# Optimization experiments

Hardware: AMD Instinct MI355X
Metric: run time of the kernel (lower is better)

The kernel has to match this reference:

```python
import jax, jax.numpy as jnp
import numpy as np

E = 128  # embed_size


def setup_inputs() -> dict:
    key = jax.random.key(0)
    ks = jax.random.split(key, 20)
    NU, NI, NEV = 100000, 50000, 4096
    s = 0.05  # weight scale so softplus(dot) stays well-conditioned
    inp = {
        "user_emb": jax.random.normal(ks[0], (NU, E), jnp.float32) * s,
        "item_emb": jax.random.normal(ks[1], (NI, E), jnp.float32) * s,
        "ugru_wi": jax.random.normal(ks[2], (3 * E, E), jnp.float32) * s,
        "ugru_wh": jax.random.normal(ks[3], (3 * E, E), jnp.float32) * s,
        "ugru_bi": jax.random.normal(ks[4], (3 * E,), jnp.float32) * s,
        "ugru_bh": jax.random.normal(ks[5], (3 * E,), jnp.float32) * s,
        "igru_wi": jax.random.normal(ks[6], (3 * E, E), jnp.float32) * s,
        "igru_wh": jax.random.normal(ks[7], (3 * E, E), jnp.float32) * s,
        "igru_bi": jax.random.normal(ks[8], (3 * E,), jnp.float32) * s,
        "igru_bh": jax.random.normal(ks[9], (3 * E,), jnp.float32) * s,
        "t1_w": jax.random.normal(ks[10], (E, 2 * E), jnp.float32) * s,
        "t1_b": jax.random.normal(ks[11], (E,), jnp.float32) * s,
        "t2_w": jax.random.normal(ks[12], (32, E), jnp.float32) * s,
        "t2_b": jax.random.normal(ks[13], (32,), jnp.float32) * s,
        "t3_w": jax.random.normal(ks[14], (1, 32), jnp.float32) * s,
        "t3_b": jax.random.normal(ks[15], (1,), jnp.float32) * s,
        "user_ids": jax.random.randint(ks[16], (NEV,), 0, NU, jnp.int32),
        "item_ids": jax.random.randint(ks[17], (NEV,), 0, NI, jnp.int32),
    }
    return inp


def _gru(x, h, wi, wh, bi, bh):
    # torch.nn.GRUCell math, single sample: x,h [E]; wi,wh [3E,E]
    gi = wi @ x + bi
    gh = wh @ h + bh
    ir, iz, inn = jnp.split(gi, 3)
    hr, hz, hn = jnp.split(gh, 3)
    r = jax.nn.sigmoid(ir + hr)
    z = jax.nn.sigmoid(iz + hz)
    n = jnp.tanh(inn + r * hn)
    return (1.0 - z) * n + z * h


def reference(user_emb, item_emb, ugru_wi, ugru_wh, ugru_bi, ugru_bh,
              igru_wi, igru_wh, igru_bi, igru_bh,
              t1_w, t1_b, t2_w, t2_b, t3_w, t3_b,
              user_ids, item_ids):
    # Sequential event processing: per-event gather of user/item embedding,
    # Rayleigh base compatibility score, MLP (transForm1/2/3) branch score,
    # coupled GRUCell updates scattered back into the embedding tables.
    def step(carry, ev):
        U, V = carry
        u_id, i_id = ev
        u = U[u_id]          # [E] gather (dict-cache lookup in original)
        v = V[i_id]          # [E]
        comp = jax.nn.softplus(jnp.dot(u, v)) + 1e-10  # base_compatibility
        loss = -jnp.log(comp)                           # -log p(event)
        cat = jnp.concatenate([u, v])                   # [2E]
        h = jax.nn.relu(t1_w @ cat + t1_b)              # transForm1 + act
        h = jax.nn.relu(t2_w @ h + t2_b)                # transForm2 + act
        score = jax.nn.sigmoid(t3_w @ h + t3_b)[0]      # transForm3
        nu = _gru(v, u, ugru_wi, ugru_wh, ugru_bi, ugru_bh)  # user_cell
        nv = _gru(u, v, igru_wi, igru_wh, igru_bi, igru_bh)  # item_cell
        U = U.at[u_id].set(nu)  # coevolution scatter
        V = V.at[i_id].set(nv)
        return (U, V), jnp.stack([loss, score])

    (_, _), outs = jax.lax.scan(step, (user_emb, item_emb),
                                (user_ids, item_ids))
    return outs  # [num_events, 2] : (-log comp, branch score)
```

## Files before the change

kernel.cpp:

```cpp
#include <hip/hip_runtime.h>
#include <math.h>

#define EMB 128
#define MAXEV 4096
#define GEV 16

struct Hdr { int nl0; int nl1; int ncomp2; };

typedef __attribute__((ext_vector_type(8))) short bf16x8;
typedef __attribute__((ext_vector_type(4))) float f32x4;

__device__ __forceinline__ float sigmoidf_(float x) { return 1.0f / (1.0f + expf(-x)); }
__device__ __forceinline__ float softplusf_(float x) {
    return (x > 0.f) ? x + log1pf(expf(-x)) : log1pf(expf(x));
}
__device__ __forceinline__ unsigned short f2bf(float f) {
    unsigned int u = __float_as_uint(f);
    u += 0x7FFFu + ((u >> 16) & 1u);
    return (unsigned short)(u >> 16);
}
__device__ __forceinline__ float bf2f(unsigned short s) {
    return __uint_as_float((unsigned int)s << 16);
}

__global__ __launch_bounds__(64) void prev_kernel(
    const int* __restrict__ uids, const int* __restrict__ iids,
    int* __restrict__ prevu, int* __restrict__ previ, int nev)
{
    int t = blockIdx.x;
    if (t >= nev) return;
    int lane = threadIdx.x;
    int myu = uids[t], myi = iids[t];
    int bu = -1, bi = -1;
    for (int j = lane; j < t; j += 64) {
        if (uids[j] == myu) bu = j;
        if (iids[j] == myi) bi = j;
    }
    for (int off = 32; off; off >>= 1) {
        bu = max(bu, __shfl_xor(bu, off));
        bi = max(bi, __shfl_xor(bi, off));
    }
    if (lane == 0) { prevu[t] = bu; previ[t] = bi; }
}

__global__ __launch_bounds__(1024) void setup_kernel(
    const int* __restrict__ prevu, const int* __restrict__ previ,
    int* __restrict__ order0, int* __restrict__ order1,
    int* __restrict__ tail2Order, int* __restrict__ compStart,
    Hdr* __restrict__ hdr, int nev)
{
    __shared__ int   lab[MAXEV];
    __shared__ int   tmpT[MAXEV];
    __shared__ int   skey[MAXEV];
    __shared__ short slev[MAXEV];
    __shared__ int   schanged, sn0, sn1, sn2;

    int tid = threadIdx.x;
    for (int t = tid; t < nev; t += 1024) { lab[t] = t; slev[t] = 0; }
    if (tid == 0) { sn0 = 0; sn1 = 0; sn2 = 0; }
    __syncthreads();

    for (int it = 0; it < nev; ++it) {
        if (tid == 0) schanged = 0;
        __syncthreads();
        for (int t = tid; t < nev; t += 1024) {
            int pu = prevu[t], pi = previ[t];
            int nl = 0;
            if (pu >= 0) nl = slev[pu] + 1;
            if (pi >= 0) { int c = slev[pi] + 1; nl = nl > c ? nl : c; }
            if (nl > (int)slev[t]) { slev[t] = (short)nl; schanged = 1; }
        }
        __syncthreads();
        if (!schanged) break;
        __syncthreads();
    }

    for (int it = 0; it < nev; ++it) {
        if (tid == 0) schanged = 0;
        __syncthreads();
        for (int t = tid; t < nev; t += 1024) {
            int m = lab[t];
            int pu = prevu[t], pi = previ[t];
            if (pu >= 0) m = min(m, lab[pu]);
            if (pi >= 0) m = min(m, lab[pi]);
            if (m < lab[t]) { atomicMin(&lab[t], m); schanged = 1; }
            if (pu >= 0 && m < lab[pu]) { atomicMin(&lab[pu], m); schanged = 1; }
            if (pi >= 0 && m < lab[pi]) { atomicMin(&lab[pi], m); schanged = 1; }
        }
        __syncthreads();
        if (!schanged) break;
        __syncthreads();
    }

    for (int t = tid; t < nev; t += 1024) {
        int l = slev[t];
        if (l == 0)      order0[atomicAdd(&sn0, 1)] = t;
        else if (l == 1) order1[atomicAdd(&sn1, 1)] = t;
        else             tmpT[atomicAdd(&sn2, 1)] = t;
    }
    __syncthreads();
    int n2 = sn2;

    for (int i = tid; i < n2; i += 1024)
        skey[i] = (lab[tmpT[i]] << 12) | tmpT[i];
    __syncthreads();

    for (int i = tid; i < n2; i += 1024) {
        int k = skey[i], r = 0;
        for (int j = 0; j < n2; ++j) r += (skey[j] < k);
        tail2Order[r] = tmpT[i];
        lab[r] = k;
    }
    __syncthreads();

    if (tid == 0) {
        int nc = 0;
        for (int i = 0; i < n2; ++i)
            if (i == 0 || (lab[i] >> 12) != (lab[i - 1] >> 12))
                compStart[nc++] = i;
        compStart[nc] = n2;
        hdr->nl0 = sn0;
        hdr->nl1 = sn1;
        hdr->ncomp2 = nc;
    }
}

__global__ __launch_bounds__(256) void wcvt_kernel(
    const float* __restrict__ Wuh, const float* __restrict__ Wii,
    const float* __restrict__ Wui, const float* __restrict__ Wih,
    const float* __restrict__ T1w,
    unsigned short* __restrict__ wb_uh, unsigned short* __restrict__ wb_ii,
    unsigned short* __restrict__ wb_ui, unsigned short* __restrict__ wb_ih,
    unsigned short* __restrict__ t1wb)
{
    int m = blockIdx.y;
    const float* src = (m == 0) ? Wuh : (m == 1) ? Wii : (m == 2) ? Wui
                      : (m == 3) ? Wih : T1w;
    unsigned short* dst = (m == 0) ? wb_uh : (m == 1) ? wb_ii : (m == 2) ? wb_ui
                        : (m == 3) ? wb_ih : t1wb;
    int nf4 = (m < 4) ? (384 * EMB / 4) : (EMB * 256 / 4);
    int q = blockIdx.x * 256 + threadIdx.x;
    if (q >= nf4) return;
    float4 v = ((const float4*)src)[q];
    ushort4 o = make_ushort4(f2bf(v.x), f2bf(v.y), f2bf(v.z), f2bf(v.w));
    *(ushort4*)(dst + (size_t)q * 4) = o;
}

__global__ __launch_bounds__(256) void gru_fused_kernel(
    const float* __restrict__ U0, const float* __restrict__ V0,
    const unsigned short* __restrict__ wb_ui, const unsigned short* __restrict__ wb_uh,
    const unsigned short* __restrict__ wb_ii, const unsigned short* __restrict__ wb_ih,
    const float* __restrict__ bui, const float* __restrict__ buh,
    const float* __restrict__ bii, const float* __restrict__ bih,
    const int* __restrict__ uids, const int* __restrict__ iids,
    const int* __restrict__ prevu, const int* __restrict__ previ,
    const float* NUr, const float* NVr,
    const int* __restrict__ order, const int* __restrict__ cnt_p,
    float* NU, float* NV)
{
    __shared__ __align__(16) unsigned short xbu[GEV][EMB];
    __shared__ __align__(16) unsigned short xbv[GEV][EMB];
    __shared__ float gg[GEV][772];

    int cnt = *cnt_p;
    int e0 = blockIdx.x * GEV;
    if (e0 >= cnt) return;

    int tid = threadIdx.x;
    int ev = tid >> 4, c8 = (tid & 15) * 8;

    {
        int e = e0 + ev;
        float4 a0, a1, c0, c1;
        if (e < cnt) {
            int t = order[e];
            int pu = prevu[t], pi = previ[t];
            const float* up = (pu < 0 ? U0 + (size_t)uids[t] * EMB : NUr + (size_t)pu * EMB) + c8;
            const float* vp = (pi < 0 ? V0 + (size_t)iids[t] * EMB : NVr + (size_t)pi * EMB) + c8;
            a0 = ((const float4*)up)[0]; a1 = ((const float4*)up)[1];
            c0 = ((const float4*)vp)[0]; c1 = ((const float4*)vp)[1];
        } else {
            a0 = make_float4(0.f, 0.f, 0.f, 0.f); a1 = a0; c0 = a0; c1 = a0;
        }
        *(ushort4*)&xbu[ev][c8]     = make_ushort4(f2bf(a0.x), f2bf(a0.y), f2bf(a0.z), f2bf(a0.w));
        *(ushort4*)&xbu[ev][c8 + 4] = make_ushort4(f2bf(a1.x), f2bf(a1.y), f2bf(a1.z), f2bf(a1.w));
        *(ushort4*)&xbv[ev][c8]     = make_ushort4(f2bf(c0.x), f2bf(c0.y), f2bf(c0.z), f2bf(c0.w));
        *(ushort4*)&xbv[ev][c8 + 4] = make_ushort4(f2bf(c1.x), f2bf(c1.y), f2bf(c1.z), f2bf(c1.w));
    }
    __syncthreads();

    int w = tid >> 6, l = tid & 63;
    int lr = l & 15, lk = (l >> 4) * 8;

    for (int ph = 0; ph < 2; ++ph) {
        const unsigned short* Wi = ph ? wb_ii : wb_ui;
        const unsigned short* Wh = ph ? wb_ih : wb_uh;
        const unsigned short (*Xi)[EMB] = ph ? xbu : xbv;
        const unsigned short (*Xh)[EMB] = ph ? xbv : xbu;

        f32x4 acc[12] = {};
        #pragma unroll
        for (int kk = 0; kk < 4; ++kk) {
            bf16x8 ai = *(const bf16x8*)&Xi[lr][kk * 32 + lk];
            bf16x8 ah = *(const bf16x8*)&Xh[lr][kk * 32 + lk];
            #pragma unroll
            for (int j = 0; j < 12; ++j) {
                int nt = w * 12 + j;
                bool ish = nt >= 24;
                int brow = (ish ? nt - 24 : nt) * 16 + lr;
                const unsigned short* W = ish ? Wh : Wi;
                bf16x8 b = *(const bf16x8*)(W + (size_t)brow * EMB + kk * 32 + lk);
                acc[j] = __builtin_amdgcn_mfma_f32_16x16x32_bf16(ish ? ah : ai, b, acc[j], 0, 0, 0);
            }
        }
        #pragma unroll
        for (int j = 0; j < 12; ++j) {
            int nt = w * 12 + j;
            #pragma unroll
            for (int i = 0; i < 4; ++i)
                gg[(l >> 4) * 4 + i][nt * 16 + lr] = acc[j][i];
        }
        __syncthreads();

        {
            int e = e0 + ev;
            if (e < cnt) {
                int t = order[e];
                const float* bi = ph ? bii : bui;
                const float* bh = ph ? bih : buh;
                float* N = ph ? NV : NU;
                const unsigned short (*xh)[EMB] = ph ? xbv : xbu;
                #pragma unroll
                for (int i = 0; i < 8; ++i) {
                    int ch = c8 + i;
                    float r_ = sigmoidf_(gg[ev][ch] + bi[ch] + gg[ev][384 + ch] + bh[ch]);
                    float z_ = sigmoidf_(gg[ev][128 + ch] + bi[128 + ch] + gg[ev][512 + ch] + bh[128 + ch]);
                    float n_ = tanhf(gg[ev][256 + ch] + bi[256 + ch] + r_ * (gg[ev][640 + ch] + bh[256 + ch]));
                    float h = bf2f(xh[ev][ch]);
                    N[(size_t)t * EMB + ch] = (1.f - z_) * n_ + z_ * h;
                }
            }
        }
        __syncthreads();
    }
}

__global__ __launch_bounds__(1024) void tail2_kernel(
    const float* __restrict__ U0,  const float* __restrict__ V0,
    const float* __restrict__ Wui, const float* __restrict__ Wuh,
    const float* __restrict__ bui, const float* __restrict__ buh,
    const float* __restrict__ Wii, const float* __restrict__ Wih,
    const float* __restrict__ bii, const float* __restrict__ bih,
    const int* __restrict__ uids,  const int* __restrict__ iids,
    const int* __restrict__ prevu, const int* __restrict__ previ,
    const int* __restrict__ tail2Order, const int* __restrict__ compStart,
    const Hdr* __restrict__ hdr,
    float* __restrict__ NU, float* __restrict__ NV)
{
    __shared__ __align__(16) float su[EMB];
    __shared__ __align__(16) float sv[EMB];
    __shared__ float gg[1536];
    int tid = threadIdx.x;
    int ncomp = hdr->ncomp2;

    int g = tid >> 4, j = tid & 15;
    int mat = g >> 4;
    const float* W = (mat == 0) ? Wui : (mat == 1) ? Wuh : (mat == 2) ? Wii : Wih;

    for (int c = blockIdx.x; c < ncomp; c += gridDim.x) {
        int kb = compStart[c], ke = compStart[c + 1];
        for (int k = kb; k < ke; ++k) {
            int t = tail2Order[k];
            int pu = prevu[t], pi = previ[t];
            const float* up = (pu < 0) ? U0 + (size_t)uids[t] * EMB : NU + (size_t)pu * EMB;
            const float* vp = (pi < 0) ? V0 + (size_t)iids[t] * EMB : NV + (size_t)pi * EMB;
            __syncthreads();
            if (tid < EMB)        su[tid] = up[tid];
            else if (tid < 2*EMB) sv[tid - EMB] = vp[tid - EMB];
            __syncthreads();

            const float* x = (mat == 1 || mat == 2) ? su : sv;
            const float4* x4 = (const float4*)x;
            float4 xa = x4[2 * j], xb = x4[2 * j + 1];
            #pragma unroll 1
            for (int b = 0; b < 3; ++b) {
                int rbase = (g & 15) * 24 + b * 8;
                float4 w0[8], w1[8];
                #pragma unroll
                for (int q = 0; q < 8; ++q) {
                    const float4* W4 = (const float4*)(W + (size_t)(rbase + q) * EMB);
                    w0[q] = W4[2 * j]; w1[q] = W4[2 * j + 1];
                }
                #pragma unroll
                for (int q = 0; q < 8; ++q) {
                    float s = w0[q].x * xa.x + w0[q].y * xa.y
                            + w0[q].z * xa.z + w0[q].w * xa.w
                            + w1[q].x * xb.x + w1[q].y * xb.y
                            + w1[q].z * xb.z + w1[q].w * xb.w;
                    s += __shfl_xor(s, 1); s += __shfl_xor(s, 2);
                    s += __shfl_xor(s, 4); s += __shfl_xor(s, 8);
                    if (j == q) gg[mat * 384 + rbase + q] = s;
                }
            }
            __syncthreads();

            if (tid < EMB) {
                int e = tid;
                float r_ = sigmoidf_(gg[e] + bui[e] + gg[384 + e] + buh[e]);
                float z_ = sigmoidf_(gg[128 + e] + bui[128 + e] + gg[512 + e] + buh[128 + e]);
                float n_ = tanhf(gg[256 + e] + bui[256 + e] + r_ * (gg[640 + e] + buh[256 + e]));
                NU[(size_t)t * EMB + e] = (1.f - z_) * n_ + z_ * su[e];
            } else if (tid < 2*EMB) {
                int e = tid - EMB;
                float r_ = sigmoidf_(gg[768 + e] + bii[e] + gg[1152 + e] + bih[e]);
                float z_ = sigmoidf_(gg[896 + e] + bii[128 + e] + gg[1280 + e] + bih[128 + e]);
                float n_ = tanhf(gg[1024 + e] + bii[256 + e] + r_ * (gg[1408 + e] + bih[256 + e]));
                NV[(size_t)t * EMB + e] = (1.f - z_) * n_ + z_ * sv[e];
            }
        }
    }
}

__global__ __launch_bounds__(256) void gatherall_kernel(
    const float* __restrict__ U0, const float* __restrict__ V0,
    const int* __restrict__ uids, const int* __restrict__ iids,
    const int* __restrict__ prevu, const int* __restrict__ previ,
    const float* __restrict__ NU, const float* __restrict__ NV,
    unsigned short* __restrict__ XAub, unsigned short* __restrict__ XAvb,
    float* __restrict__ out, int nev)
{
    int sub = threadIdx.x >> 5;
    int lane = threadIdx.x & 31;
    int t = blockIdx.x * 8 + sub;
    if (t >= nev) return;
    int pu = prevu[t], pi = previ[t];
    const float4* up = (const float4*)(pu < 0 ?
        U0 + (size_t)uids[t] * EMB : NU + (size_t)pu * EMB);
    const float4* vp = (const float4*)(pi < 0 ?
        V0 + (size_t)iids[t] * EMB : NV + (size_t)pi * EMB);
    float4 a = up[lane], c = vp[lane];
    *(ushort4*)(XAub + (size_t)t * EMB + lane * 4) =
        make_ushort4(f2bf(a.x), f2bf(a.y), f2bf(a.z), f2bf(a.w));
    *(ushort4*)(XAvb + (size_t)t * EMB + lane * 4) =
        make_ushort4(f2bf(c.x), f2bf(c.y), f2bf(c.z), f2bf(c.w));
    float dp = a.x * c.x + a.y * c.y + a.z * c.z + a.w * c.w;
    dp += __shfl_xor(dp, 1); dp += __shfl_xor(dp, 2);
    dp += __shfl_xor(dp, 4); dp += __shfl_xor(dp, 8);
    dp += __shfl_xor(dp, 16);
    if (lane == 0) out[2 * (size_t)t] = -logf(softplusf_(dp) + 1e-10f);
}

__global__ __launch_bounds__(256) void t1_mfma_kernel(
    const unsigned short* __restrict__ XAub, const unsigned short* __restrict__ XAvb,
    const unsigned short* __restrict__ t1wb, const float* __restrict__ T1b,
    float* __restrict__ H1, int nev)
{
    int ev0 = blockIdx.x * 64;
    int row0 = blockIdx.y * 64;
    int tid = threadIdx.x;
    int w = tid >> 6, l = tid & 63;
    int lr = l & 15, lk = (l >> 4) * 8;
    int erow = ev0 + w * 16 + lr;

    f32x4 acc[4] = {};
    #pragma unroll
    for (int kh = 0; kh < 8; ++kh) {
        const unsigned short* Xb = (kh < 4) ? XAub : XAvb;
        bf16x8 a = *(const bf16x8*)(Xb + (size_t)erow * EMB + (kh & 3) * 32 + lk);
        #pragma unroll
        for (int n = 0; n < 4; ++n) {
            bf16x8 b = *(const bf16x8*)(t1wb + (size_t)(row0 + n * 16 + lr) * 256 + kh * 32 + lk);
            acc[n] = __builtin_amdgcn_mfma_f32_16x16x32_bf16(a, b, acc[n], 0, 0, 0);
        }
    }
    int drow = ev0 + w * 16 + (l >> 4) * 4;
    #pragma unroll
    for (int n = 0; n < 4; ++n) {
        int col = row0 + n * 16 + lr;
        float bb = T1b[col];
        #pragma unroll
        for (int i = 0; i < 4; ++i)
            H1[(size_t)(drow + i) * EMB + col] = fmaxf(acc[n][i] + bb, 0.f);
    }
}

__global__ __launch_bounds__(256) void t2t3_kernel(
    const float* __restrict__ H1,
    const float* __restrict__ T2w, const float* __restrict__ T2b,
    const float* __restrict__ T3w, const float* __restrict__ T3b,
    float* __restrict__ out, int nev)
{
    __shared__ __align__(16) float w2s[32][132];
    __shared__ __align__(16) float h1s[16][132];
    __shared__ float h2s[16][36];
    int tid = threadIdx.x;
    int ev = tid >> 4, j = tid & 15;
    int t = blockIdx.x * 16 + ev;

    {
        const float4* s2 = (const float4*)T2w;
        #pragma unroll
        for (int i = 0; i < 4; ++i) {
            int q = i * 256 + tid;
            int r = q >> 5, c4 = q & 31;
            *(float4*)&w2s[r][c4 * 4] = s2[q];
        }
    }
    {
        const float4* h4 = (const float4*)(H1 + (size_t)(blockIdx.x * 16 + ev) * EMB);
        *(float4*)&h1s[ev][8 * j]     = h4[2 * j];
        *(float4*)&h1s[ev][8 * j + 4] = h4[2 * j + 1];
    }
    __syncthreads();

    float acc0 = T2b[2 * j], acc1 = T2b[2 * j + 1];
    const float4* wr0 = (const float4*)&w2s[2 * j][0];
    const float4* wr1 = (const float4*)&w2s[2 * j + 1][0];
    const float4* xh = (const float4*)&h1s[ev][0];
    #pragma unroll
    for (int k = 0; k < 32; ++k) {
        float4 x = xh[k], a = wr0[k], b = wr1[k];
        acc0 = fmaf(a.x, x.x, acc0); acc0 = fmaf(a.y, x.y, acc0);
        acc0 = fmaf(a.z, x.z, acc0); acc0 = fmaf(a.w, x.w, acc0);
        acc1 = fmaf(b.x, x.x, acc1); acc1 = fmaf(b.y, x.y, acc1);
        acc1 = fmaf(b.z, x.z, acc1); acc1 = fmaf(b.w, x.w, acc1);
    }
    h2s[ev][2 * j]     = fmaxf(acc0, 0.f);
    h2s[ev][2 * j + 1] = fmaxf(acc1, 0.f);
    __syncthreads();

    float p = T3w[2 * j] * h2s[ev][2 * j] + T3w[2 * j + 1] * h2s[ev][2 * j + 1];
    p += __shfl_xor(p, 1); p += __shfl_xor(p, 2);
    p += __shfl_xor(p, 4); p += __shfl_xor(p, 8);
    if (j == 0 && t < nev)
        out[2 * (size_t)t + 1] = sigmoidf_(p + T3b[0]);
}

extern "C" void kernel_launch(void* const* d_in, const int* in_sizes, int n_in,
                              void* d_out, int out_size, void* d_ws, size_t ws_size,
                              hipStream_t stream)
{
    const float* U0  = (const float*)d_in[0];
    const float* V0  = (const float*)d_in[1];
    const float* Wui = (const float*)d_in[2];
    const float* Wuh = (const float*)d_in[3];
    const float* bui = (const float*)d_in[4];
    const float* buh = (const float*)d_in[5];
    const float* Wii = (const float*)d_in[6];
    const float* Wih = (const float*)d_in[7];
    const float* bii = (const float*)d_in[8];
    const float* bih = (const float*)d_in[9];
    const float* T1w = (const float*)d_in[10];
    const float* T1b = (const float*)d_in[11];
    const float* T2w = (const float*)d_in[12];
    const float* T2b = (const float*)d_in[13];
    const float* T3w = (const float*)d_in[14];
    const float* T3b = (const float*)d_in[15];
    const int* uids  = (const int*)d_in[16];
    const int* iids  = (const int*)d_in[17];
    int nev = in_sizes[16];

    char* ws = (char*)d_ws;
    int* base = (int*)ws;
    int* prevu      = base;
    int* previ      = base + MAXEV;
    int* order0     = base + 2 * MAXEV;
    int* order1     = base + 3 * MAXEV;
    int* tail2Order = base + 4 * MAXEV;
    int* compStart  = base + 5 * MAXEV;
    Hdr* hdr        = (Hdr*)(base + 6 * MAXEV + 4);
    float* NU = (float*)(ws + (160 << 10));
    float* NV = NU + (size_t)MAXEV * EMB;
    float* Xu = NV + (size_t)MAXEV * EMB;
    float* Xv = Xu + (size_t)MAXEV * EMB;
    float* Gu = Xv + (size_t)MAXEV * EMB;
    float* Gv = Gu + (size_t)MAXEV * 768;
    unsigned short* Xub = (unsigned short*)(Gv + (size_t)MAXEV * 768);
    unsigned short* Xvb = Xub + (size_t)MAXEV * EMB;
    unsigned short* wb_uh = Xvb + (size_t)MAXEV * EMB;
    unsigned short* wb_ii = wb_uh + 384 * EMB;
    unsigned short* wb_ui = wb_ii + 384 * EMB;
    unsigned short* wb_ih = wb_ui + 384 * EMB;
    unsigned short* t1wb  = wb_ih + 384 * EMB;
    float* out = (float*)d_out;

    prev_kernel<<<nev, 64, 0, stream>>>(uids, iids, prevu, previ, nev);
    wcvt_kernel<<<dim3(48, 5), 256, 0, stream>>>(
        Wuh, Wii, Wui, Wih, T1w, wb_uh, wb_ii, wb_ui, wb_ih, t1wb);
    setup_kernel<<<1, 1024, 0, stream>>>(prevu, previ, order0, order1,
                                         tail2Order, compStart, hdr, nev);

    gru_fused_kernel<<<MAXEV / GEV, 256, 0, stream>>>(
        U0, V0, wb_ui, wb_uh, wb_ii, wb_ih, bui, buh, bii, bih,
        uids, iids, prevu, previ, NU, NV, order0, &hdr->nl0, NU, NV);

    gru_fused_kernel<<<MAXEV / GEV, 256, 0, stream>>>(
        U0, V0, wb_ui, wb_uh, wb_ii, wb_ih, bui, buh, bii, bih,
        uids, iids, prevu, previ, NU, NV, order1, &hdr->nl1, NU, NV);

    tail2_kernel<<<64, 1024, 0, stream>>>(
        U0, V0, Wui, Wuh, bui, buh, Wii, Wih, bii, bih,
        uids, iids, prevu, previ, tail2Order, compStart, hdr, NU, NV);

    unsigned short* XAub = Xub;
    unsigned short* XAvb = Xvb;
    float* H1 = Gu;
    gatherall_kernel<<<(nev + 7) / 8, 256, 0, stream>>>(
        U0, V0, uids, iids, prevu, previ, NU, NV, XAub, XAvb, out, nev);
    t1_mfma_kernel<<<dim3((nev + 63) / 64, 2), 256, 0, stream>>>(
        XAub, XAvb, t1wb, T1b, H1, nev);
    t2t3_kernel<<<(nev + 15) / 16, 256, 0, stream>>>(
        H1, T2w, T2b, T3w, T3b, out, nev);
}
```

Before: 122.6 us.

## Fuse weight conversion into prev kernel, fuse post MLP kernels, prune setup work

Weight bf16 conversion, now including T2w, is folded into prev_kernel, which removes one launch. The gather, T1 MFMA, T2 and T3 stages become a single post_fused_kernel that keeps activations in LDS and uses MFMA for T2, so the H1 and X round trips through global memory go away. setup_kernel now runs level propagation only over events that have predecessors and labelling only over tail events, and it drops one shared array. GRU LDS rows are padded to 136 to reduce bank conflicts. T2 now runs in bf16, which trades some precision for speed.

```diff
diff --git a/kernel.cpp b/kernel.cpp
--- a/kernel.cpp
+++ b/kernel.cpp
@@ -25,11 +25,34 @@
 
 __global__ __launch_bounds__(64) void prev_kernel(
     const int* __restrict__ uids, const int* __restrict__ iids,
-    int* __restrict__ prevu, int* __restrict__ previ, int nev)
+    int* __restrict__ prevu, int* __restrict__ previ, int nev,
+    const float* __restrict__ Wuh, const float* __restrict__ Wii,
+    const float* __restrict__ Wui, const float* __restrict__ Wih,
+    const float* __restrict__ T1w, const float* __restrict__ T2w,
+    unsigned short* __restrict__ wb_uh, unsigned short* __restrict__ wb_ii,
+    unsigned short* __restrict__ wb_ui, unsigned short* __restrict__ wb_ih,
+    unsigned short* __restrict__ t1wb, unsigned short* __restrict__ t2wb)
 {
     int t = blockIdx.x;
+    int lane = threadIdx.x;
+
+    {
+        int gid = t * 64 + lane;
+        if (gid < 58368) {
+            const float* src; unsigned short* dst; int q;
+            if (gid < 49152) {
+                int m = gid / 12288; q = gid - m * 12288;
+                src = (m == 0) ? Wuh : (m == 1) ? Wii : (m == 2) ? Wui : Wih;
+                dst = (m == 0) ? wb_uh : (m == 1) ? wb_ii : (m == 2) ? wb_ui : wb_ih;
+            } else if (gid < 57344) { q = gid - 49152; src = T1w; dst = t1wb; }
+            else                    { q = gid - 57344; src = T2w; dst = t2wb; }
+            float4 v = ((const float4*)src)[q];
+            *(ushort4*)(dst + (size_t)q * 4) =
+                make_ushort4(f2bf(v.x), f2bf(v.y), f2bf(v.z), f2bf(v.w));
+        }
+    }
+
     if (t >= nev) return;
-    int lane = threadIdx.x;
     int myu = uids[t], myi = iids[t];
     int bu = -1, bi = -1;
     for (int j = lane; j < t; j += 64) {
@@ -51,19 +74,27 @@
 {
     __shared__ int   lab[MAXEV];
     __shared__ int   tmpT[MAXEV];
-    __shared__ int   skey[MAXEV];
+    __shared__ int   t2l[MAXEV];
     __shared__ short slev[MAXEV];
-    __shared__ int   schanged, sn0, sn1, sn2;
+    __shared__ int   schanged, sn0, sn1, sn2, sntl;
 
     int tid = threadIdx.x;
-    for (int t = tid; t < nev; t += 1024) { lab[t] = t; slev[t] = 0; }
-    if (tid == 0) { sn0 = 0; sn1 = 0; sn2 = 0; }
-    __syncthreads();
+    for (int t = tid; t < nev; t += 1024) slev[t] = 0;
+    if (tid == 0) { sn0 = 0; sn1 = 0; sn2 = 0; sntl = 0; }
+    __syncthreads();
+
+    for (int t = tid; t < nev; t += 1024) {
+        if (prevu[t] >= 0 || previ[t] >= 0) tmpT[atomicAdd(&sntl, 1)] = t;
+        else                                 order0[atomicAdd(&sn0, 1)] = t;
+    }
+    __syncthreads();
+    int ntl = sntl;
 
     for (int it = 0; it < nev; ++it) {
         if (tid == 0) schanged = 0;
         __syncthreads();
-        for (int t = tid; t < nev; t += 1024) {
+        for (int i = tid; i < ntl; i += 1024) {
+            int t = tmpT[i];
             int pu = prevu[t], pi = previ[t];
             int nl = 0;
             if (pu >= 0) nl = slev[pu] + 1;
@@ -75,75 +106,55 @@
         __syncthreads();
     }
 
+    for (int i = tid; i < ntl; i += 1024) {
+        int t = tmpT[i];
+        if (slev[t] == 1)      order1[atomicAdd(&sn1, 1)] = t;
+        else if (slev[t] >= 2) t2l[atomicAdd(&sn2, 1)] = t;
+    }
+    __syncthreads();
+    int n2 = sn2;
+
+    for (int i = tid; i < n2; i += 1024) lab[t2l[i]] = t2l[i];
+    __syncthreads();
     for (int it = 0; it < nev; ++it) {
         if (tid == 0) schanged = 0;
         __syncthreads();
-        for (int t = tid; t < nev; t += 1024) {
+        for (int i = tid; i < n2; i += 1024) {
+            int t = t2l[i];
             int m = lab[t];
             int pu = prevu[t], pi = previ[t];
-            if (pu >= 0) m = min(m, lab[pu]);
-            if (pi >= 0) m = min(m, lab[pi]);
+            bool eu = (pu >= 0 && slev[pu] >= 2);
+            bool ei = (pi >= 0 && slev[pi] >= 2);
+            if (eu) m = min(m, lab[pu]);
+            if (ei) m = min(m, lab[pi]);
             if (m < lab[t]) { atomicMin(&lab[t], m); schanged = 1; }
-            if (pu >= 0 && m < lab[pu]) { atomicMin(&lab[pu], m); schanged = 1; }
-            if (pi >= 0 && m < lab[pi]) { atomicMin(&lab[pi], m); schanged = 1; }
+            if (eu && m < lab[pu]) { atomicMin(&lab[pu], m); schanged = 1; }
+            if (ei && m < lab[pi]) { atomicMin(&lab[pi], m); schanged = 1; }
         }
         __syncthreads();
         if (!schanged) break;
         __syncthreads();
     }
 
-    for (int t = tid; t < nev; t += 1024) {
-        int l = slev[t];
-        if (l == 0)      order0[atomicAdd(&sn0, 1)] = t;
-        else if (l == 1) order1[atomicAdd(&sn1, 1)] = t;
-        else             tmpT[atomicAdd(&sn2, 1)] = t;
-    }
-    __syncthreads();
-    int n2 = sn2;
-
-    for (int i = tid; i < n2; i += 1024)
-        skey[i] = (lab[tmpT[i]] << 12) | tmpT[i];
-    __syncthreads();
-
+    for (int i = tid; i < n2; i += 1024) tmpT[i] = (lab[t2l[i]] << 12) | t2l[i];
+    __syncthreads();
     for (int i = tid; i < n2; i += 1024) {
-        int k = skey[i], r = 0;
-        for (int j = 0; j < n2; ++j) r += (skey[j] < k);
-        tail2Order[r] = tmpT[i];
-        lab[r] = k;
+        int k = tmpT[i], r = 0;
+        for (int j = 0; j < n2; ++j) r += (tmpT[j] < k);
+        tail2Order[r] = k & 0xFFF;
     }
     __syncthreads();
 
     if (tid == 0) {
         int nc = 0;
         for (int i = 0; i < n2; ++i)
-            if (i == 0 || (lab[i] >> 12) != (lab[i - 1] >> 12))
+            if (i == 0 || lab[tail2Order[i]] != lab[tail2Order[i - 1]])
                 compStart[nc++] = i;
         compStart[nc] = n2;
+        hdr->ncomp2 = nc;
         hdr->nl0 = sn0;
         hdr->nl1 = sn1;
-        hdr->ncomp2 = nc;
-    }
-}
-
-__global__ __launch_bounds__(256) void wcvt_kernel(
-    const float* __restrict__ Wuh, const float* __restrict__ Wii,
-    const float* __restrict__ Wui, const float* __restrict__ Wih,
-    const float* __restrict__ T1w,
-    unsigned short* __restrict__ wb_uh, unsigned short* __restrict__ wb_ii,
-    unsigned short* __restrict__ wb_ui, unsigned short* __restrict__ wb_ih,
-    unsigned short* __restrict__ t1wb)
-{
-    int m = blockIdx.y;
-    const float* src = (m == 0) ? Wuh : (m == 1) ? Wii : (m == 2) ? Wui
-                      : (m == 3) ? Wih : T1w;
-    unsigned short* dst = (m == 0) ? wb_uh : (m == 1) ? wb_ii : (m == 2) ? wb_ui
-                        : (m == 3) ? wb_ih : t1wb;
-    int nf4 = (m < 4) ? (384 * EMB / 4) : (EMB * 256 / 4);
-    int q = blockIdx.x * 256 + threadIdx.x;
-    if (q >= nf4) return;
-    float4 v = ((const float4*)src)[q];
-    ushort4 o = make_ushort4(f2bf(v.x), f2bf(v.y), f2bf(v.z), f2bf(v.w));
-    *(ushort4*)(dst + (size_t)q * 4) = o;
+    }
 }
 
 __global__ __launch_bounds__(256) void gru_fused_kernel(
@@ -158,8 +169,8 @@
     const int* __restrict__ order, const int* __restrict__ cnt_p,
     float* NU, float* NV)
 {
-    __shared__ __align__(16) unsigned short xbu[GEV][EMB];
-    __shared__ __align__(16) unsigned short xbv[GEV][EMB];
+    __shared__ __align__(16) unsigned short xbu[GEV][136];
+    __shared__ __align__(16) unsigned short xbv[GEV][136];
     __shared__ float gg[GEV][772];
 
     int cnt = *cnt_p;
@@ -195,8 +206,8 @@
     for (int ph = 0; ph < 2; ++ph) {
         const unsigned short* Wi = ph ? wb_ii : wb_ui;
         const unsigned short* Wh = ph ? wb_ih : wb_uh;
-        const unsigned short (*Xi)[EMB] = ph ? xbu : xbv;
-        const unsigned short (*Xh)[EMB] = ph ? xbv : xbu;
+        const unsigned short (*Xi)[136] = ph ? xbu : xbv;
+        const unsigned short (*Xh)[136] = ph ? xbv : xbu;
 
         f32x4 acc[12] = {};
         #pragma unroll
@@ -229,7 +240,7 @@
                 const float* bi = ph ? bii : bui;
                 const float* bh = ph ? bih : buh;
                 float* N = ph ? NV : NU;
-                const unsigned short (*xh)[EMB] = ph ? xbv : xbu;
+                const unsigned short (*xh)[136] = ph ? xbv : xbu;
                 #pragma unroll
                 for (int i = 0; i < 8; ++i) {
                     int ch = c8 + i;
@@ -321,119 +332,115 @@
     }
 }
 
-__global__ __launch_bounds__(256) void gatherall_kernel(
+__global__ __launch_bounds__(256) void post_fused_kernel(
     const float* __restrict__ U0, const float* __restrict__ V0,
     const int* __restrict__ uids, const int* __restrict__ iids,
     const int* __restrict__ prevu, const int* __restrict__ previ,
     const float* __restrict__ NU, const float* __restrict__ NV,
-    unsigned short* __restrict__ XAub, unsigned short* __restrict__ XAvb,
-    float* __restrict__ out, int nev)
-{
-    int sub = threadIdx.x >> 5;
-    int lane = threadIdx.x & 31;
-    int t = blockIdx.x * 8 + sub;
-    if (t >= nev) return;
-    int pu = prevu[t], pi = previ[t];
-    const float4* up = (const float4*)(pu < 0 ?
-        U0 + (size_t)uids[t] * EMB : NU + (size_t)pu * EMB);
-    const float4* vp = (const float4*)(pi < 0 ?
-        V0 + (size_t)iids[t] * EMB : NV + (size_t)pi * EMB);
-    float4 a = up[lane], c = vp[lane];
-    *(ushort4*)(XAub + (size_t)t * EMB + lane * 4) =
-        make_ushort4(f2bf(a.x), f2bf(a.y), f2bf(a.z), f2bf(a.w));
-    *(ushort4*)(XAvb + (size_t)t * EMB + lane * 4) =
-        make_ushort4(f2bf(c.x), f2bf(c.y), f2bf(c.z), f2bf(c.w));
-    float dp = a.x * c.x + a.y * c.y + a.z * c.z + a.w * c.w;
-    dp += __shfl_xor(dp, 1); dp += __shfl_xor(dp, 2);
-    dp += __shfl_xor(dp, 4); dp += __shfl_xor(dp, 8);
-    dp += __shfl_xor(dp, 16);
-    if (lane == 0) out[2 * (size_t)t] = -logf(softplusf_(dp) + 1e-10f);
-}
-
-__global__ __launch_bounds__(256) void t1_mfma_kernel(
-    const unsigned short* __restrict__ XAub, const unsigned short* __restrict__ XAvb,
     const unsigned short* __restrict__ t1wb, const float* __restrict__ T1b,
-    float* __restrict__ H1, int nev)
-{
-    int ev0 = blockIdx.x * 64;
-    int row0 = blockIdx.y * 64;
-    int tid = threadIdx.x;
-    int w = tid >> 6, l = tid & 63;
-    int lr = l & 15, lk = (l >> 4) * 8;
-    int erow = ev0 + w * 16 + lr;
-
-    f32x4 acc[4] = {};
-    #pragma unroll
-    for (int kh = 0; kh < 8; ++kh) {
-        const unsigned short* Xb = (kh < 4) ? XAub : XAvb;
-        bf16x8 a = *(const bf16x8*)(Xb + (size_t)erow * EMB + (kh & 3) * 32 + lk);
-        #pragma unroll
-        for (int n = 0; n < 4; ++n) {
-            bf16x8 b = *(const bf16x8*)(t1wb + (size_t)(row0 + n * 16 + lr) * 256 + kh * 32 + lk);
-            acc[n] = __builtin_amdgcn_mfma_f32_16x16x32_bf16(a, b, acc[n], 0, 0, 0);
-        }
-    }
-    int drow = ev0 + w * 16 + (l >> 4) * 4;
-    #pragma unroll
-    for (int n = 0; n < 4; ++n) {
-        int col = row0 + n * 16 + lr;
-        float bb = T1b[col];
-        #pragma unroll
-        for (int i = 0; i < 4; ++i)
-            H1[(size_t)(drow + i) * EMB + col] = fmaxf(acc[n][i] + bb, 0.f);
-    }
-}
-
-__global__ __launch_bounds__(256) void t2t3_kernel(
-    const float* __restrict__ H1,
-    const float* __restrict__ T2w, const float* __restrict__ T2b,
+    const unsigned short* __restrict__ t2wb, const float* __restrict__ T2b,
     const float* __restrict__ T3w, const float* __restrict__ T3b,
     float* __restrict__ out, int nev)
 {
-    __shared__ __align__(16) float w2s[32][132];
-    __shared__ __align__(16) float h1s[16][132];
-    __shared__ float h2s[16][36];
+    __shared__ __align__(16) unsigned short xau[64][136];
+    __shared__ __align__(16) unsigned short xav[64][136];
+    __shared__ __align__(16) unsigned short h1b[64][136];
+    __shared__ float h2s[64][36];
+
     int tid = threadIdx.x;
-    int ev = tid >> 4, j = tid & 15;
-    int t = blockIdx.x * 16 + ev;
+    int ev0 = blockIdx.x * 64;
+
+    #pragma unroll
+    for (int rep = 0; rep < 4; ++rep) {
+        int idx = rep * 256 + tid;
+        int evl = idx >> 4, j16 = idx & 15;
+        int t = ev0 + evl;
+        float4 a0, a1, c0, c1;
+        if (t < nev) {
+            int pu = prevu[t], pi = previ[t];
+            const float* up = (pu < 0 ? U0 + (size_t)uids[t] * EMB : NU + (size_t)pu * EMB) + j16 * 8;
+            const float* vp = (pi < 0 ? V0 + (size_t)iids[t] * EMB : NV + (size_t)pi * EMB) + j16 * 8;
+            a0 = ((const float4*)up)[0]; a1 = ((const float4*)up)[1];
+            c0 = ((const float4*)vp)[0]; c1 = ((const float4*)vp)[1];
+        } else {
+            a0 = make_float4(0.f, 0.f, 0.f, 0.f); a1 = a0; c0 = a0; c1 = a0;
+        }
+        *(ushort4*)&xau[evl][j16 * 8]     = make_ushort4(f2bf(a0.x), f2bf(a0.y), f2bf(a0.z), f2bf(a0.w));
+        *(ushort4*)&xau[evl][j16 * 8 + 4] = make_ushort4(f2bf(a1.x), f2bf(a1.y), f2bf(a1.z), f2bf(a1.w));
+        *(ushort4*)&xav[evl][j16 * 8]     = make_ushort4(f2bf(c0.x), f2bf(c0.y), f2bf(c0.z), f2bf(c0.w));
+        *(ushort4*)&xav[evl][j16 * 8 + 4] = make_ushort4(f2bf(c1.x), f2bf(c1.y), f2bf(c1.z), f2bf(c1.w));
+        float dp = a0.x * c0.x + a0.y * c0.y + a0.z * c0.z + a0.w * c0.w
+                 + a1.x * c1.x + a1.y * c1.y + a1.z * c1.z + a1.w * c1.w;
+        dp += __shfl_xor(dp, 1); dp += __shfl_xor(dp, 2);
+        dp += __shfl_xor(dp, 4); dp += __shfl_xor(dp, 8);
+        if (j16 == 0 && t < nev)
+            out[2 * (size_t)t] = -logf(softplusf_(dp) + 1e-10f);
+    }
+    __syncthreads();
+
+    int w = tid >> 6, l = tid & 63;
+    int lr = l & 15, lk = (l >> 4) * 8;
 
     {
-        const float4* s2 = (const float4*)T2w;
-        #pragma unroll
-        for (int i = 0; i < 4; ++i) {
-            int q = i * 256 + tid;
-            int r = q >> 5, c4 = q & 31;
-            *(float4*)&w2s[r][c4 * 4] = s2[q];
-        }
-    }
+        f32x4 acc[8] = {};
+        #pragma unroll
+        for (int kh = 0; kh < 8; ++kh) {
+            const unsigned short* ar = (kh < 4)
+                ? &xau[w * 16 + lr][kh * 32 + lk]
+                : &xav[w * 16 + lr][(kh - 4) * 32 + lk];
+            bf16x8 a = *(const bf16x8*)ar;
+            #pragma unroll
+            for (int n = 0; n < 8; ++n) {
+                bf16x8 b = *(const bf16x8*)(t1wb + (size_t)(n * 16 + lr) * 256 + kh * 32 + lk);
+                acc[n] = __builtin_amdgcn_mfma_f32_16x16x32_bf16(a, b, acc[n], 0, 0, 0);
+            }
+        }
+        #pragma unroll
+        for (int n = 0; n < 8; ++n) {
+            int col = n * 16 + lr;
+            float bb = T1b[col];
+            #pragma unroll
+            for (int i = 0; i < 4; ++i)
+                h1b[w * 16 + (l >> 4) * 4 + i][col] = f2bf(fmaxf(acc[n][i] + bb, 0.f));
+        }
+    }
+    __syncthreads();
+
     {
-        const float4* h4 = (const float4*)(H1 + (size_t)(blockIdx.x * 16 + ev) * EMB);
-        *(float4*)&h1s[ev][8 * j]     = h4[2 * j];
-        *(float4*)&h1s[ev][8 * j + 4] = h4[2 * j + 1];
-    }
-    __syncthreads();
-
-    float acc0 = T2b[2 * j], acc1 = T2b[2 * j + 1];
-    const float4* wr0 = (const float4*)&w2s[2 * j][0];
-    const float4* wr1 = (const float4*)&w2s[2 * j + 1][0];
-    const float4* xh = (const float4*)&h1s[ev][0];
-    #pragma unroll
-    for (int k = 0; k < 32; ++k) {
-        float4 x = xh[k], a = wr0[k], b = wr1[k];
-        acc0 = fmaf(a.x, x.x, acc0); acc0 = fmaf(a.y, x.y, acc0);
-        acc0 = fmaf(a.z, x.z, acc0); acc0 = fmaf(a.w, x.w, acc0);
-        acc1 = fmaf(b.x, x.x, acc1); acc1 = fmaf(b.y, x.y, acc1);
-        acc1 = fmaf(b.z, x.z, acc1); acc1 = fmaf(b.w, x.w, acc1);
-    }
-    h2s[ev][2 * j]     = fmaxf(acc0, 0.f);
-    h2s[ev][2 * j + 1] = fmaxf(acc1, 0.f);
-    __syncthreads();
-
-    float p = T3w[2 * j] * h2s[ev][2 * j] + T3w[2 * j + 1] * h2s[ev][2 * j + 1];
-    p += __shfl_xor(p, 1); p += __shfl_xor(p, 2);
-    p += __shfl_xor(p, 4); p += __shfl_xor(p, 8);
-    if (j == 0 && t < nev)
-        out[2 * (size_t)t + 1] = sigmoidf_(p + T3b[0]);
+        f32x4 acc2[2] = {};
+        #pragma unroll
+        for (int kk = 0; kk < 4; ++kk) {
+            bf16x8 a = *(const bf16x8*)&h1b[w * 16 + lr][kk * 32 + lk];
+            #pragma unroll
+            for (int n = 0; n < 2; ++n) {
+                bf16x8 b = *(const bf16x8*)(t2wb + (size_t)(n * 16 + lr) * 128 + kk * 32 + lk);
+                acc2[n] = __builtin_amdgcn_mfma_f32_16x16x32_bf16(a, b, acc2[n], 0, 0, 0);
+            }
+        }
+        #pragma unroll
+        for (int n = 0; n < 2; ++n) {
+            int col = n * 16 + lr;
+            float bb = T2b[col];
+            #pragma unroll
+            for (int i = 0; i < 4; ++i)
+                h2s[w * 16 + (l >> 4) * 4 + i][col] = fmaxf(acc2[n][i] + bb, 0.f);
+        }
+    }
+    __syncthreads();
+
+    {
+        int evl = tid >> 2, q4 = tid & 3;
+        float p = 0.f;
+        #pragma unroll
+        for (int i = 0; i < 8; ++i) {
+            int ch = q4 * 8 + i;
+            p = fmaf(T3w[ch], h2s[evl][ch], p);
+        }
+        p += __shfl_xor(p, 1); p += __shfl_xor(p, 2);
+        int t = ev0 + evl;
+        if (q4 == 0 && t < nev)
+            out[2 * (size_t)t + 1] = sigmoidf_(p + T3b[0]);
+    }
 }
 
 extern "C" void kernel_launch(void* const* d_in, const int* in_sizes, int n_in,
@@ -471,22 +478,18 @@
     Hdr* hdr        = (Hdr*)(base + 6 * MAXEV + 4);
     float* NU = (float*)(ws + (160 << 10));
     float* NV = NU + (size_t)MAXEV * EMB;
-    float* Xu = NV + (size_t)MAXEV * EMB;
-    float* Xv = Xu + (size_t)MAXEV * EMB;
-    float* Gu = Xv + (size_t)MAXEV * EMB;
-    float* Gv = Gu + (size_t)MAXEV * 768;
-    unsigned short* Xub = (unsigned short*)(Gv + (size_t)MAXEV * 768);
-    unsigned short* Xvb = Xub + (size_t)MAXEV * EMB;
-    unsigned short* wb_uh = Xvb + (size_t)MAXEV * EMB;
+    unsigned short* wb_uh = (unsigned short*)(NV + (size_t)MAXEV * EMB);
     unsigned short* wb_ii = wb_uh + 384 * EMB;
     unsigned short* wb_ui = wb_ii + 384 * EMB;
     unsigned short* wb_ih = wb_ui + 384 * EMB;
     unsigned short* t1wb  = wb_ih + 384 * EMB;
+    unsigned short* t2wb  = t1wb + EMB * 256;
     float* out = (float*)d_out;
 
-    prev_kernel<<<nev, 64, 0, stream>>>(uids, iids, prevu, previ, nev);
-    wcvt_kernel<<<dim3(48, 5), 256, 0, stream>>>(
-        Wuh, Wii, Wui, Wih, T1w, wb_uh, wb_ii, wb_ui, wb_ih, t1wb);
+    prev_kernel<<<MAXEV, 64, 0, stream>>>(
+        uids, iids, prevu, previ, nev,
+        Wuh, Wii, Wui, Wih, T1w, T2w,
+        wb_uh, wb_ii, wb_ui, wb_ih, t1wb, t2wb);
     setup_kernel<<<1, 1024, 0, stream>>>(prevu, previ, order0, order1,
                                          tail2Order, compStart, hdr, nev);
 
@@ -502,13 +505,7 @@
         U0, V0, Wui, Wuh, bui, buh, Wii, Wih, bii, bih,
         uids, iids, prevu, previ, tail2Order, compStart, hdr, NU, NV);
 
-    unsigned short* XAub = Xub;
-    unsigned short* XAvb = Xvb;
-    float* H1 = Gu;
-    gatherall_kernel<<<(nev + 7) / 8, 256, 0, stream>>>(
-        U0, V0, uids, iids, prevu, previ, NU, NV, XAub, XAvb, out, nev);
-    t1_mfma_kernel<<<dim3((nev + 63) / 64, 2), 256, 0, stream>>>(
-        XAub, XAvb, t1wb, T1b, H1, nev);
-    t2t3_kernel<<<(nev + 15) / 16, 256, 0, stream>>>(
-        H1, T2w, T2b, T3w, T3b, out, nev);
-}
+    post_fused_kernel<<<(nev + 63) / 64, 256, 0, stream>>>(
+        U0, V0, uids, iids, prevu, previ, NU, NV,
+        t1wb, T1b, t2wb, T2b, T3w, T3b, out, nev);
+}
```

Measured after the change: 107.3 us. 12.5% less time.
